# Kernel optimization log

Measured on AMD Instinct MI355X. Metric: run time of the kernel, lower is better.

Reference implementation:

```python
import jax, jax.numpy as jnp
import numpy as np

H, DH = 16, 64          # num_heads, dim_head
DIM = 1024              # dim_ltn
EPS = 1e-5


def setup_inputs() -> dict:
    key = jax.random.key(0)
    ks = jax.random.split(key, 8)
    b, n_txt, t, m = 2, 2048, 4, 256
    text = jax.random.normal(ks[0], (b, n_txt, DIM), dtype=jnp.float32)
    image = jax.random.normal(ks[1], (b, t, m, DIM), dtype=jnp.float32)
    locations = jax.random.randint(ks[2], (b, n_txt), 0, 2)  # 0/1 media markers
    s = DIM ** -0.5
    Wq = jax.random.normal(ks[3], (DIM, H * DH), dtype=jnp.float32) * s
    Wkv = jax.random.normal(ks[4], (DIM, 2 * H * DH), dtype=jnp.float32) * s
    Wo = jax.random.normal(ks[5], (H * DH, DIM), dtype=jnp.float32) * s
    ln_gamma = jnp.ones((DIM,), dtype=jnp.float32)
    ln_beta = jnp.zeros((DIM,), dtype=jnp.float32)
    return {"text": text, "image": image, "locations": locations,
            "Wq": Wq, "Wkv": Wkv, "Wo": Wo,
            "ln_gamma": ln_gamma, "ln_beta": ln_beta}


def reference(text, image, locations, Wq, Wkv, Wo, ln_gamma, ln_beta):
    scale = DH ** -0.5
    b, t, m, d = image.shape
    # LayerNorm(text)
    mu = text.mean(-1, keepdims=True)
    var = ((text - mu) ** 2).mean(-1, keepdims=True)
    tn = (text - mu) / jnp.sqrt(var + EPS) * ln_gamma + ln_beta
    img = image.reshape(b, t * m, d)             # b (t m) d
    q = tn @ Wq                                  # b n (h dh)
    k, v = jnp.split(img @ Wkv, 2, axis=-1)      # each b tm (h dh)
    split_heads = lambda x: x.reshape(x.shape[0], x.shape[1], H, DH).transpose(0, 2, 1, 3)
    q, k, v = split_heads(q), split_heads(k), split_heads(v)
    attn = jnp.einsum('bhid,bhjd->bhij', q, k) * scale   # b h n (t m)
    txt_time = jnp.cumsum(locations, axis=-1)            # b n : media index per text token
    viz_time = jnp.repeat(jnp.arange(1, t + 1), m)       # (t m)
    # only_attend_to_immediate -> equality mask
    mask = txt_time[:, None, :, None] == viz_time[None, None, None, :]
    neg = -jnp.finfo(attn.dtype).max
    attn = jnp.where(mask, attn, neg)
    attn = jax.nn.softmax(attn, axis=-1)
    # zero attention for text tokens before any media (txt_time == 0)
    attn = jnp.where((txt_time == 0)[:, None, :, None], 0.0, attn)
    out = jnp.einsum('bhij,bhjd->bhid', attn, v)
    out = out.transpose(0, 2, 1, 3).reshape(b, -1, H * DH)
    return out @ Wo
```

## Files before the change

kernel.cpp:

```cpp
#include <hip/hip_runtime.h>

#define BATCH 2
#define NTXT  2048
#define TMED  4
#define MMED  256
#define TM    (TMED * MMED)
#define DIM   1024
#define NH    16
#define DHD   64
#define KVW   2048
#define RMAX  256
#define RT    32

typedef _Float16 f16x8 __attribute__((ext_vector_type(8)));
typedef float    f32x4 __attribute__((ext_vector_type(4)));

#define GLOAD_LDS16(g, l)                                                  \
  __builtin_amdgcn_global_load_lds(                                        \
      (const __attribute__((address_space(1))) unsigned int*)(g),          \
      (__attribute__((address_space(3))) unsigned int*)(l), 16, 0, 0)

__global__ __launch_bounds__(1024) void k1_scan_cvt_tr(
    const int* __restrict__ loc, const float* __restrict__ image,
    const float* __restrict__ Wkv, int* __restrict__ tt, int* __restrict__ seg,
    float* __restrict__ ipart, _Float16* __restrict__ img16,
    _Float16* __restrict__ WkvT) {
  __shared__ int buf[NTXT];
  __shared__ int s_start, s_end;
  __shared__ float tile[64][65];
  const int idx = blockIdx.x;
  const int tid = threadIdx.x;
  if (idx < BATCH) {
    const int b = idx;
    if (tid == 0) { s_start = NTXT; s_end = NTXT; }
    buf[tid]        = loc[b * NTXT + tid];
    buf[tid + 1024] = loc[b * NTXT + tid + 1024];
    __syncthreads();
    for (int off = 1; off < NTXT; off <<= 1) {
      int a0 = (tid >= off) ? buf[tid - off] : 0;
      int a1 = buf[tid + 1024 - off];
      __syncthreads();
      buf[tid] += a0;
      buf[tid + 1024] += a1;
      __syncthreads();
    }
    const int v0 = buf[tid], v1 = buf[tid + 1024];
    tt[b * NTXT + tid]        = v0;
    tt[b * NTXT + tid + 1024] = v1;
    if (v0 >= 1) atomicMin(&s_start, tid);
    if (v0 >= 5) atomicMin(&s_end, tid);
    if (v1 >= 1) atomicMin(&s_start, tid + 1024);
    if (v1 >= 5) atomicMin(&s_end, tid + 1024);
    __syncthreads();
    if (tid == 0) {
      seg[b * 2]     = s_start;
      seg[b * 2 + 1] = s_end - s_start;
    }
  } else if (idx < BATCH + 256) {
    const int j = idx - BATCH;
    const int b = j >> 7, rt = j & 127;
    const size_t base = (size_t)(b * TM + rt * 8) * DIM + tid;
    const float* p = image + base;
    _Float16* q = img16 + base;
    float s = 0.f;
#pragma unroll
    for (int r = 0; r < 8; r++) {
      const float v = p[(size_t)r * DIM];
      s += v;
      q[(size_t)r * DIM] = (_Float16)v;
    }
    ipart[(size_t)(b * 128 + rt) * DIM + tid] = s;
  } else {
    const int j2 = idx - BATCH - 256;
    const int k0 = (j2 & 15) * 64, n0 = (j2 >> 4) * 64;
    const int r = tid >> 4, c4 = (tid & 15) * 4;
    const float4 v = *reinterpret_cast<const float4*>(
        Wkv + (size_t)(k0 + r) * KVW + n0 + c4);
    tile[r][c4 + 0] = v.x; tile[r][c4 + 1] = v.y;
    tile[r][c4 + 2] = v.z; tile[r][c4 + 3] = v.w;
    __syncthreads();
    if (tid < 512) {
      const int n = tid >> 3, kc = (tid & 7) * 8;
      f16x8 h;
#pragma unroll
      for (int u = 0; u < 8; u++) h[u] = (_Float16)tile[kc + u][n];
      *reinterpret_cast<f16x8*>(WkvT + (size_t)(n0 + n) * DIM + k0 + kc) = h;
    }
  }
}

__global__ __launch_bounds__(256) void k2_prep(
    const float* __restrict__ Wkv, const float* __restrict__ text,
    const float* __restrict__ gamma, const float* __restrict__ beta,
    const int* __restrict__ seg, const float* __restrict__ ipart,
    float* __restrict__ tn, float* __restrict__ vbar) {
  __shared__ float red[256];
  const int idx = blockIdx.x;
  const int tid = threadIdx.x;
  if (idx < 64) {
    const int b = idx >> 5, rt = idx & 31;
    const int i0 = seg[b * 2];
    const int cnt = min(seg[b * 2 + 1], RMAX);
    for (int r = rt; r < cnt; r += RT) {
      const float* xrow = text + (size_t)(b * NTXT + i0 + r) * DIM;
      float x[4];
      float s = 0.f;
#pragma unroll
      for (int u = 0; u < 4; u++) { x[u] = xrow[tid + 256 * u]; s += x[u]; }
      red[tid] = s; __syncthreads();
      for (int st = 128; st > 0; st >>= 1) {
        if (tid < st) red[tid] += red[tid + st];
        __syncthreads();
      }
      const float mu = red[0] * (1.0f / DIM); __syncthreads();
      float vs = 0.f;
#pragma unroll
      for (int u = 0; u < 4; u++) { float d = x[u] - mu; vs += d * d; }
      red[tid] = vs; __syncthreads();
      for (int st = 128; st > 0; st >>= 1) {
        if (tid < st) red[tid] += red[tid + st];
        __syncthreads();
      }
      const float rstd = rsqrtf(red[0] * (1.0f / DIM) + 1e-5f); __syncthreads();
      float* trow = tn + (size_t)(b * RMAX + r) * DIM;
#pragma unroll
      for (int u = 0; u < 4; u++) {
        const int c = tid + 256 * u;
        trow[c] = (x[u] - mu) * rstd * gamma[c] + beta[c];
      }
      __syncthreads();
    }
  } else {
    const int j = idx - 64;
    const int b = j >> 5, et = (j >> 3) & 3, cc = j & 7;
    const int e = et * 256 + tid;
    const int c0 = cc * 128;
    if (tid < 128) {
      float s = 0.f;
      for (int p = 0; p < 128; p++)
        s += ipart[(size_t)(b * 128 + p) * DIM + c0 + tid];
      red[tid] = s * (1.0f / (float)TM);
    }
    __syncthreads();
    float s = 0.f;
    for (int c = 0; c < 128; c++)
      s += red[c] * Wkv[(size_t)(c0 + c) * KVW + DIM + e];
    atomicAdd(&vbar[b * DIM + e], s);
  }
}

__global__ __launch_bounds__(256) void k3_gemm_qproj_obar(
    const _Float16* __restrict__ img16, const _Float16* __restrict__ WkvT,
    const float* __restrict__ Wq, const float* __restrict__ Wo,
    const float* __restrict__ tn, const float* __restrict__ vbar,
    const int* __restrict__ seg, _Float16* __restrict__ kv16,
    float* __restrict__ qbuf, float* __restrict__ obar) {
  __shared__ __align__(16) char smem[16384];
  const int idx = blockIdx.x;
  const int tid = threadIdx.x;
  if (idx < 256) {
    _Float16* As = (_Float16*)smem;
    _Float16* Bs = As + 128 * 32;
    const int swz = (idx & 7) * 32 + (idx >> 3);
    const int lane = tid & 63, wid = tid >> 6;
    const int wm = wid & 1, wn = wid >> 1;
    const int row0 = (swz >> 4) * 128, col0 = (swz & 15) * 128;
    const int frow = lane & 15, fq = lane >> 4;
    const int srow = lane >> 2, skc = (lane & 3) * 8;
    f32x4 acc[4][4] = {};
    for (int k0 = 0; k0 < DIM; k0 += 32) {
      __syncthreads();
#pragma unroll
      for (int i = 0; i < 2; i++) {
        const int ci = wid * 2 + i;
        const int r = ci * 16 + srow;
        GLOAD_LDS16(img16 + (size_t)(row0 + r) * DIM + k0 + skc,
                    As + ci * 512);
        GLOAD_LDS16(WkvT + (size_t)(col0 + r) * DIM + k0 + skc,
                    Bs + ci * 512);
      }
      __syncthreads();
      f16x8 af[4], bf[4];
#pragma unroll
      for (int mt = 0; mt < 4; mt++)
        af[mt] = *reinterpret_cast<const f16x8*>(
            As + (wm * 64 + mt * 16 + frow) * 32 + fq * 8);
#pragma unroll
      for (int nt = 0; nt < 4; nt++)
        bf[nt] = *reinterpret_cast<const f16x8*>(
            Bs + (wn * 64 + nt * 16 + frow) * 32 + fq * 8);
#pragma unroll
      for (int mt = 0; mt < 4; mt++)
#pragma unroll
        for (int nt = 0; nt < 4; nt++)
          acc[mt][nt] = __builtin_amdgcn_mfma_f32_16x16x32_f16(
              af[mt], bf[nt], acc[mt][nt], 0, 0, 0);
    }
#pragma unroll
    for (int mt = 0; mt < 4; mt++)
#pragma unroll
      for (int nt = 0; nt < 4; nt++) {
        const int col = col0 + wn * 64 + nt * 16 + frow;
#pragma unroll
        for (int r = 0; r < 4; r++) {
          const int row = row0 + wm * 64 + mt * 16 + fq * 4 + r;
          kv16[(size_t)row * KVW + col] = (_Float16)acc[mt][nt][r];
        }
      }
  } else if (idx < 320) {
    float* tn_s = (float*)smem;
    const int j = idx - 256;
    const int b = j >> 5, nt = (j >> 2) & 7, cc = j & 3;
    const int n0 = nt * 128, c0 = cc * 256;
    const int n = tid & 127, cs = tid >> 7;
    const int cnt = min(seg[b * 2 + 1], RMAX);
    for (int r0 = 0; r0 < cnt; r0 += 8) {
      const int rows = min(8, cnt - r0);
      for (int i = tid; i < 8 * 256; i += 256) {
        const int r = i >> 8, c = i & 255;
        tn_s[i] = (r < rows) ? tn[(size_t)(b * RMAX + r0 + r) * DIM + c0 + c]
                             : 0.f;
      }
      __syncthreads();
      float acc[8] = {};
      for (int ci = 0; ci < 128; ci++) {
        const int c = cs * 128 + ci;
        const float w = Wq[(size_t)(c0 + c) * DIM + n0 + n];
#pragma unroll
        for (int rr = 0; rr < 8; rr++) acc[rr] += tn_s[rr * 256 + c] * w;
      }
      for (int rr = 0; rr < rows; rr++)
        atomicAdd(&qbuf[(size_t)(b * RMAX + r0 + rr) * DIM + n0 + n], acc[rr]);
      __syncthreads();
    }
  } else {
    float* vb_s = (float*)smem;
    const int j = idx - 320;
    const int b = j >> 5, et = (j >> 3) & 3, cc = j & 7;
    const int e = et * 256 + tid;
    const int c0 = cc * 128;
    if (tid < 128) vb_s[tid] = vbar[b * DIM + c0 + tid];
    __syncthreads();
    float s = 0.f;
    for (int c = 0; c < 128; c++)
      s += vb_s[c] * Wo[(size_t)(c0 + c) * DIM + e];
    atomicAdd(&obar[b * DIM + e], s);
  }
}

__global__ __launch_bounds__(256) void k4_fill_attn(
    const float* __restrict__ text, const _Float16* __restrict__ kv16,
    const float* __restrict__ Wq, const float* __restrict__ Wo,
    const float* __restrict__ gamma, const float* __restrict__ beta,
    const int* __restrict__ tt, const int* __restrict__ seg,
    const float* __restrict__ obar, const float* __restrict__ qbuf,
    float* __restrict__ oacc, float* __restrict__ out) {
  __shared__ float red[256];
  __shared__ float pbuf[256];
  const int idx = blockIdx.x;
  const int tid = threadIdx.x;
  if (idx < BATCH * NTXT) {
    const int b = idx >> 11;
    const int i = idx & (NTXT - 1);
    const int t = tt[b * NTXT + i];
    float* orow = out + (size_t)(b * NTXT + i) * DIM;
    if (t == 0) {
      for (int c = tid; c < DIM; c += 256) orow[c] = 0.f;
      return;
    }
    if (t > TMED) {
      const float* ob = obar + b * DIM;
      for (int c = tid; c < DIM; c += 256) orow[c] = ob[c];
      return;
    }
    if (i - seg[b * 2] < RMAX) return;
    __shared__ float tns[DIM];
    __shared__ float qrow[DIM];
    __shared__ float oaccs[DIM];
    const float* xrow = text + (size_t)(b * NTXT + i) * DIM;
    float x[4];
    float s = 0.f;
#pragma unroll
    for (int u = 0; u < 4; u++) { x[u] = xrow[tid + 256 * u]; s += x[u]; }
    red[tid] = s; __syncthreads();
    for (int st = 128; st > 0; st >>= 1) {
      if (tid < st) red[tid] += red[tid + st];
      __syncthreads();
    }
    const float mu = red[0] * (1.0f / DIM); __syncthreads();
    float vs = 0.f;
#pragma unroll
    for (int u = 0; u < 4; u++) { float d = x[u] - mu; vs += d * d; }
    red[tid] = vs; __syncthreads();
    for (int st = 128; st > 0; st >>= 1) {
      if (tid < st) red[tid] += red[tid + st];
      __syncthreads();
    }
    const float rstd = rsqrtf(red[0] * (1.0f / DIM) + 1e-5f); __syncthreads();
#pragma unroll
    for (int u = 0; u < 4; u++) {
      const int c = tid + 256 * u;
      tns[c] = (x[u] - mu) * rstd * gamma[c] + beta[c];
    }
    __syncthreads();
    {
      float qa[4] = {0.f, 0.f, 0.f, 0.f};
      for (int c = 0; c < DIM; c++) {
        const float tv = tns[c];
        const float* w = Wq + (size_t)c * DIM + tid;
#pragma unroll
        for (int u = 0; u < 4; u++) qa[u] += tv * w[256 * u];
      }
#pragma unroll
      for (int u = 0; u < 4; u++) qrow[tid + 256 * u] = qa[u];
    }
    __syncthreads();
    const size_t kvrow0 = (size_t)(b * TM + (t - 1) * MMED) * KVW;
    const int d0 = tid & 63, g = tid >> 6;
    for (int h = 0; h < NH; h++) {
      const _Float16* krow = kv16 + kvrow0 + (size_t)tid * KVW + h * DHD;
      float sc = 0.f;
#pragma unroll
      for (int d = 0; d < DHD; d++) sc += qrow[h * DHD + d] * (float)krow[d];
      sc *= 0.125f;
      red[tid] = sc; __syncthreads();
      for (int st = 128; st > 0; st >>= 1) {
        if (tid < st) red[tid] = fmaxf(red[tid], red[tid + st]);
        __syncthreads();
      }
      const float mx = red[0]; __syncthreads();
      const float e = __expf(sc - mx);
      red[tid] = e; __syncthreads();
      for (int st = 128; st > 0; st >>= 1) {
        if (tid < st) red[tid] += red[tid + st];
        __syncthreads();
      }
      const float inv = 1.0f / red[0]; __syncthreads();
      pbuf[tid] = e * inv; __syncthreads();
      const _Float16* vbase = kv16 + kvrow0 + (size_t)(g * 64) * KVW + DIM + h * DHD + d0;
      float a = 0.f;
#pragma unroll 8
      for (int jj = 0; jj < 64; jj++) a += pbuf[g * 64 + jj] * (float)vbase[(size_t)jj * KVW];
      red[tid] = a; __syncthreads();
      if (tid < 64)
        oaccs[h * DHD + tid] = red[tid] + red[64 + tid] + red[128 + tid] + red[192 + tid];
      __syncthreads();
    }
    float oa[4] = {0.f, 0.f, 0.f, 0.f};
    for (int c = 0; c < DIM; c++) {
      const float ov = oaccs[c];
      const float* w = Wo + (size_t)c * DIM + tid;
#pragma unroll
      for (int u = 0; u < 4; u++) oa[u] += ov * w[256 * u];
    }
#pragma unroll
    for (int u = 0; u < 4; u++) orow[tid + 256 * u] = oa[u];
  } else {
    __shared__ float qs[DHD];
    const int j = idx - BATCH * NTXT;
    const int h = j & 15, rt = (j >> 4) & 31, b = j >> 9;
    const int i0 = seg[b * 2];
    const int cnt = min(seg[b * 2 + 1], RMAX);
    const int d0 = tid & 63, g = tid >> 6;
    for (int r = rt; r < cnt; r += RT) {
      const int i = i0 + r;
      const int t = tt[b * NTXT + i];
      if (tid < 64) qs[tid] = qbuf[(size_t)(b * RMAX + r) * DIM + h * DHD + tid];
      __syncthreads();
      const size_t kvrow0 = (size_t)(b * TM + (t - 1) * MMED) * KVW;
      const _Float16* krow = kv16 + kvrow0 + (size_t)tid * KVW + h * DHD;
      float sc = 0.f;
#pragma unroll
      for (int d = 0; d < DHD; d += 8) {
        const f16x8 kk = *reinterpret_cast<const f16x8*>(krow + d);
#pragma unroll
        for (int u = 0; u < 8; u++) sc += qs[d + u] * (float)kk[u];
      }
      sc *= 0.125f;
      red[tid] = sc; __syncthreads();
      for (int st = 128; st > 0; st >>= 1) {
        if (tid < st) red[tid] = fmaxf(red[tid], red[tid + st]);
        __syncthreads();
      }
      const float mx = red[0]; __syncthreads();
      const float e = __expf(sc - mx);
      red[tid] = e; __syncthreads();
      for (int st = 128; st > 0; st >>= 1) {
        if (tid < st) red[tid] += red[tid + st];
        __syncthreads();
      }
      const float inv = 1.0f / red[0]; __syncthreads();
      pbuf[tid] = e * inv; __syncthreads();
      const _Float16* vbase = kv16 + kvrow0 + (size_t)(g * 64) * KVW + DIM + h * DHD + d0;
      float a = 0.f;
#pragma unroll 8
      for (int jj = 0; jj < 64; jj++) a += pbuf[g * 64 + jj] * (float)vbase[(size_t)jj * KVW];
      red[tid] = a; __syncthreads();
      if (tid < 64)
        oacc[(size_t)(b * RMAX + r) * DIM + h * DHD + tid] =
            red[tid] + red[64 + tid] + red[128 + tid] + red[192 + tid];
      __syncthreads();
    }
  }
}

__global__ __launch_bounds__(256) void k5_oproj(
    const float* __restrict__ oacc, const float* __restrict__ Wo,
    const int* __restrict__ seg, float* __restrict__ out) {
  const int ct = blockIdx.x;
  const int rt = blockIdx.y;
  const int b = blockIdx.z;
  const int i0 = seg[b * 2];
  const int cnt = min(seg[b * 2 + 1], RMAX);
  const int tid = threadIdx.x;
  const int d0 = tid & 63, g = tid >> 6;
  __shared__ float op[4][64];
  for (int r = rt; r < cnt; r += RT) {
    const float* arow = oacc + (size_t)(b * RMAX + r) * DIM;
    const float* wo = Wo + (size_t)(g * 256) * DIM + ct * 64 + d0;
    float s = 0.f;
    for (int c = 0; c < 256; c++) s += arow[g * 256 + c] * wo[(size_t)c * DIM];
    op[g][d0] = s; __syncthreads();
    if (tid < 64)
      out[(size_t)(b * NTXT + i0 + r) * DIM + ct * 64 + tid] =
          op[0][tid] + op[1][tid] + op[2][tid] + op[3][tid];
    __syncthreads();
  }
}

extern "C" void kernel_launch(void* const* d_in, const int* in_sizes, int n_in,
                              void* d_out, int out_size, void* d_ws, size_t ws_size,
                              hipStream_t stream) {
  const float* text  = (const float*)d_in[0];
  const float* image = (const float*)d_in[1];
  const int*   loc   = (const int*)d_in[2];
  const float* Wq    = (const float*)d_in[3];
  const float* Wkv   = (const float*)d_in[4];
  const float* Wo    = (const float*)d_in[5];
  const float* gamma = (const float*)d_in[6];
  const float* beta  = (const float*)d_in[7];
  float* out = (float*)d_out;

  _Float16* kv16  = (_Float16*)d_ws;
  _Float16* WkvT  = kv16 + (size_t)BATCH * TM * KVW;
  float*    oacc  = (float*)WkvT;
  _Float16* img16 = WkvT + (size_t)KVW * DIM;
  float*    tn    = (float*)(img16 + (size_t)BATCH * TM * DIM);
  float*    qbuf  = tn + (size_t)BATCH * RMAX * DIM;
  float*    vbar  = qbuf + (size_t)BATCH * RMAX * DIM;
  float*    obar  = vbar + BATCH * DIM;
  int*      tt    = (int*)(obar + BATCH * DIM);
  int*      seg   = tt + BATCH * NTXT;
  float*    ipart = (float*)(seg + 8);

  hipMemsetAsync(qbuf, 0,
                 ((size_t)BATCH * RMAX * DIM + 2 * BATCH * DIM) * sizeof(float),
                 stream);
  k1_scan_cvt_tr<<<BATCH + 256 + 512, 1024, 0, stream>>>(
      loc, image, Wkv, tt, seg, ipart, img16, WkvT);
  k2_prep<<<128, 256, 0, stream>>>(Wkv, text, gamma, beta, seg, ipart, tn, vbar);
  k3_gemm_qproj_obar<<<384, 256, 0, stream>>>(img16, WkvT, Wq, Wo, tn, vbar,
                                              seg, kv16, qbuf, obar);
  k4_fill_attn<<<BATCH * NTXT + NH * RT * BATCH, 256, 0, stream>>>(
      text, kv16, Wq, Wo, gamma, beta, tt, seg, obar, qbuf, oacc, out);
  k5_oproj<<<dim3(16, RT, BATCH), 256, 0, stream>>>(oacc, Wo, seg, out);
}
```

Baseline: 169.1 us.

## Use 512-thread blocks in KV GEMM kernel and ballot-based segment scan

Doubles the block size of the fused GEMM/q-projection/obar kernel to 8 waves, splitting each 128x128 tile into 32-row wave slices. Global-to-LDS direct loads are replaced with register-staged vector loads, and the block swizzle is removed. The q-projection and obar branches are remapped to the larger block. Segment boundary search now uses wave ballots and a small shared reduction instead of shared atomics. The aim is more latency hiding, at the cost of more barrier overhead and fewer MFMAs per wave.

```diff
diff --git a/kernel.cpp b/kernel.cpp
--- a/kernel.cpp
+++ b/kernel.cpp
@@ -15,24 +15,18 @@
 typedef _Float16 f16x8 __attribute__((ext_vector_type(8)));
 typedef float    f32x4 __attribute__((ext_vector_type(4)));
 
-#define GLOAD_LDS16(g, l)                                                  \
-  __builtin_amdgcn_global_load_lds(                                        \
-      (const __attribute__((address_space(1))) unsigned int*)(g),          \
-      (__attribute__((address_space(3))) unsigned int*)(l), 16, 0, 0)
-
 __global__ __launch_bounds__(1024) void k1_scan_cvt_tr(
     const int* __restrict__ loc, const float* __restrict__ image,
     const float* __restrict__ Wkv, int* __restrict__ tt, int* __restrict__ seg,
     float* __restrict__ ipart, _Float16* __restrict__ img16,
     _Float16* __restrict__ WkvT) {
   __shared__ int buf[NTXT];
-  __shared__ int s_start, s_end;
   __shared__ float tile[64][65];
+  __shared__ int wmin[2][16];
   const int idx = blockIdx.x;
   const int tid = threadIdx.x;
   if (idx < BATCH) {
     const int b = idx;
-    if (tid == 0) { s_start = NTXT; s_end = NTXT; }
     buf[tid]        = loc[b * NTXT + tid];
     buf[tid + 1024] = loc[b * NTXT + tid + 1024];
     __syncthreads();
@@ -47,14 +41,30 @@
     const int v0 = buf[tid], v1 = buf[tid + 1024];
     tt[b * NTXT + tid]        = v0;
     tt[b * NTXT + tid + 1024] = v1;
-    if (v0 >= 1) atomicMin(&s_start, tid);
-    if (v0 >= 5) atomicMin(&s_end, tid);
-    if (v1 >= 1) atomicMin(&s_start, tid + 1024);
-    if (v1 >= 5) atomicMin(&s_end, tid + 1024);
+    const int lane = tid & 63, w = tid >> 6;
+    const unsigned long long b1a = __ballot(v0 >= 1);
+    const unsigned long long b1b = __ballot(v1 >= 1);
+    const unsigned long long b5a = __ballot(v0 >= 5);
+    const unsigned long long b5b = __ballot(v1 >= 5);
+    if (lane == 0) {
+      int s1 = NTXT, s5 = NTXT;
+      if (b1a)      s1 = w * 64 + (__ffsll(b1a) - 1);
+      else if (b1b) s1 = 1024 + w * 64 + (__ffsll(b1b) - 1);
+      if (b5a)      s5 = w * 64 + (__ffsll(b5a) - 1);
+      else if (b5b) s5 = 1024 + w * 64 + (__ffsll(b5b) - 1);
+      wmin[0][w] = s1;
+      wmin[1][w] = s5;
+    }
     __syncthreads();
     if (tid == 0) {
-      seg[b * 2]     = s_start;
-      seg[b * 2 + 1] = s_end - s_start;
+      int s = NTXT, e = NTXT;
+#pragma unroll
+      for (int i = 0; i < 16; i++) {
+        s = min(s, wmin[0][i]);
+        e = min(e, wmin[1][i]);
+      }
+      seg[b * 2]     = s;
+      seg[b * 2 + 1] = e - s;
     }
   } else if (idx < BATCH + 256) {
     const int j = idx - BATCH;
@@ -149,7 +159,7 @@
   }
 }
 
-__global__ __launch_bounds__(256) void k3_gemm_qproj_obar(
+__global__ __launch_bounds__(512) void k3_gemm_qproj_obar(
     const _Float16* __restrict__ img16, const _Float16* __restrict__ WkvT,
     const float* __restrict__ Wq, const float* __restrict__ Wo,
     const float* __restrict__ tn, const float* __restrict__ vbar,
@@ -161,49 +171,45 @@
   if (idx < 256) {
     _Float16* As = (_Float16*)smem;
     _Float16* Bs = As + 128 * 32;
-    const int swz = (idx & 7) * 32 + (idx >> 3);
     const int lane = tid & 63, wid = tid >> 6;
-    const int wm = wid & 1, wn = wid >> 1;
-    const int row0 = (swz >> 4) * 128, col0 = (swz & 15) * 128;
+    const int wm = wid & 3, wn = wid >> 2;
+    const int row0 = (idx >> 4) * 128, col0 = (idx & 15) * 128;
+    const int srow = tid >> 2, skc = (tid & 3) * 8;
     const int frow = lane & 15, fq = lane >> 4;
-    const int srow = lane >> 2, skc = (lane & 3) * 8;
-    f32x4 acc[4][4] = {};
+    f32x4 acc[2][4] = {};
     for (int k0 = 0; k0 < DIM; k0 += 32) {
-      __syncthreads();
-#pragma unroll
-      for (int i = 0; i < 2; i++) {
-        const int ci = wid * 2 + i;
-        const int r = ci * 16 + srow;
-        GLOAD_LDS16(img16 + (size_t)(row0 + r) * DIM + k0 + skc,
-                    As + ci * 512);
-        GLOAD_LDS16(WkvT + (size_t)(col0 + r) * DIM + k0 + skc,
-                    Bs + ci * 512);
-      }
-      __syncthreads();
-      f16x8 af[4], bf[4];
-#pragma unroll
-      for (int mt = 0; mt < 4; mt++)
+      const f16x8 av = *reinterpret_cast<const f16x8*>(
+          img16 + (size_t)(row0 + srow) * DIM + k0 + skc);
+      const f16x8 bv = *reinterpret_cast<const f16x8*>(
+          WkvT + (size_t)(col0 + srow) * DIM + k0 + skc);
+      __syncthreads();
+      *reinterpret_cast<f16x8*>(As + tid * 8) = av;
+      *reinterpret_cast<f16x8*>(Bs + tid * 8) = bv;
+      __syncthreads();
+      f16x8 af[2], bf[4];
+#pragma unroll
+      for (int mt = 0; mt < 2; mt++)
         af[mt] = *reinterpret_cast<const f16x8*>(
-            As + (wm * 64 + mt * 16 + frow) * 32 + fq * 8);
+            As + (wm * 32 + mt * 16 + frow) * 32 + fq * 8);
 #pragma unroll
       for (int nt = 0; nt < 4; nt++)
         bf[nt] = *reinterpret_cast<const f16x8*>(
             Bs + (wn * 64 + nt * 16 + frow) * 32 + fq * 8);
 #pragma unroll
-      for (int mt = 0; mt < 4; mt++)
+      for (int mt = 0; mt < 2; mt++)
 #pragma unroll
         for (int nt = 0; nt < 4; nt++)
           acc[mt][nt] = __builtin_amdgcn_mfma_f32_16x16x32_f16(
               af[mt], bf[nt], acc[mt][nt], 0, 0, 0);
     }
 #pragma unroll
-    for (int mt = 0; mt < 4; mt++)
+    for (int mt = 0; mt < 2; mt++)
 #pragma unroll
       for (int nt = 0; nt < 4; nt++) {
         const int col = col0 + wn * 64 + nt * 16 + frow;
 #pragma unroll
         for (int r = 0; r < 4; r++) {
-          const int row = row0 + wm * 64 + mt * 16 + fq * 4 + r;
+          const int row = row0 + wm * 32 + mt * 16 + fq * 4 + r;
           kv16[(size_t)row * KVW + col] = (_Float16)acc[mt][nt][r];
         }
       }
@@ -216,15 +222,15 @@
     const int cnt = min(seg[b * 2 + 1], RMAX);
     for (int r0 = 0; r0 < cnt; r0 += 8) {
       const int rows = min(8, cnt - r0);
-      for (int i = tid; i < 8 * 256; i += 256) {
+      for (int i = tid; i < 8 * 256; i += 512) {
         const int r = i >> 8, c = i & 255;
         tn_s[i] = (r < rows) ? tn[(size_t)(b * RMAX + r0 + r) * DIM + c0 + c]
                              : 0.f;
       }
       __syncthreads();
       float acc[8] = {};
-      for (int ci = 0; ci < 128; ci++) {
-        const int c = cs * 128 + ci;
+      for (int ci = 0; ci < 64; ci++) {
+        const int c = cs * 64 + ci;
         const float w = Wq[(size_t)(c0 + c) * DIM + n0 + n];
 #pragma unroll
         for (int rr = 0; rr < 8; rr++) acc[rr] += tn_s[rr * 256 + c] * w;
@@ -236,8 +242,8 @@
   } else {
     float* vb_s = (float*)smem;
     const int j = idx - 320;
-    const int b = j >> 5, et = (j >> 3) & 3, cc = j & 7;
-    const int e = et * 256 + tid;
+    const int b = j >> 4, et = (j >> 3) & 1, cc = j & 7;
+    const int e = et * 512 + tid;
     const int c0 = cc * 128;
     if (tid < 128) vb_s[tid] = vbar[b * DIM + c0 + tid];
     __syncthreads();
@@ -459,7 +465,7 @@
   k1_scan_cvt_tr<<<BATCH + 256 + 512, 1024, 0, stream>>>(
       loc, image, Wkv, tt, seg, ipart, img16, WkvT);
   k2_prep<<<128, 256, 0, stream>>>(Wkv, text, gamma, beta, seg, ipart, tn, vbar);
-  k3_gemm_qproj_obar<<<384, 256, 0, stream>>>(img16, WkvT, Wq, Wo, tn, vbar,
+  k3_gemm_qproj_obar<<<352, 512, 0, stream>>>(img16, WkvT, Wq, Wo, tn, vbar,
                                               seg, kv16, qbuf, obar);
   k4_fill_attn<<<BATCH * NTXT + NH * RT * BATCH, 256, 0, stream>>>(
       text, kv16, Wq, Wo, gamma, beta, tt, seg, obar, qbuf, oacc, out);
```

Result: faster. 153.0 us (-9.6%).
